# Optimization experiments

Hardware: AMD Instinct MI355X
Metric: run time of the kernel (lower is better)

Reference implementation:

```python
import jax, jax.numpy as jnp
import numpy as np

B, OBS, H, N = 16384, 512, 1024, 9

def setup_inputs() -> dict:
    key = jax.random.key(0)
    ks = jax.random.split(key, 12)
    s = 0.02
    return {
        "obs": jax.random.normal(ks[0], (B, OBS), jnp.float32),
        "agent_positions": jax.random.normal(ks[1], (B, N, 3), jnp.float32),
        "W1": jax.random.normal(ks[2], (OBS, H), jnp.float32) * s,
        "b1": jnp.zeros((H,), jnp.float32),
        "W2": jax.random.normal(ks[3], (H, H), jnp.float32) * s,
        "b2": jnp.zeros((H,), jnp.float32),
        "Wc1": jax.random.normal(ks[4], (H, H // 2), jnp.float32) * s,
        "bc1": jnp.zeros((H // 2,), jnp.float32),
        "Wc2": jax.random.normal(ks[5], (H // 2, 1), jnp.float32) * s,
        "bc2": jnp.zeros((1,), jnp.float32),
        "Wt1": jax.random.normal(ks[6], (H, H // 2), jnp.float32) * s,
        "bt1": jnp.zeros((H // 2,), jnp.float32),
        "Wt2": jax.random.normal(ks[7], (H // 2, 1), jnp.float32) * s,
        "bt2": jnp.zeros((1,), jnp.float32),
        "Wk1": jax.random.normal(ks[8], (2 * H, H), jnp.float32) * s,
        "bk1": jnp.zeros((H,), jnp.float32),
        "Wk2": jax.random.normal(ks[9], (H, 1), jnp.float32) * s,
        "bk2": jnp.zeros((1,), jnp.float32),
    }


def reference(obs, agent_positions, W1, b1, W2, b2, Wc1, bc1, Wc2, bc2,
              Wt1, bt1, Wt2, bt2, Wk1, bk1, Wk2, bk2):
    # global features: Linear->ReLU->Linear->ReLU
    g = jax.nn.relu(obs @ W1 + b1)
    g = jax.nn.relu(g @ W2 + b2)  # [B, H]

    # Each per-agent head is applied to the SAME g in the original loop,
    # so one pass + broadcast is mathematically identical.
    cov = jax.nn.sigmoid(jax.nn.relu(g @ Wc1 + bc1) @ Wc2 + bc2)  # [B,1]
    trk = jax.nn.sigmoid(jax.nn.relu(g @ Wt1 + bt1) @ Wt2 + bt2)  # [B,1]
    coop_in = jnp.concatenate([g, g], axis=-1)                    # [B,2H]
    coop = jax.nn.sigmoid(jax.nn.relu(coop_in @ Wk1 + bk1) @ Wk2 + bk2)  # [B,1]
    # mean over 8 identical cooperation scores == the score itself

    coverage = jnp.broadcast_to(cov, (cov.shape[0], N))      # [B, N]
    tracking = jnp.broadcast_to(trk, (trk.shape[0], N))      # [B, N]
    cooperation = jnp.broadcast_to(coop, (coop.shape[0], N)) # [B, N]
    return (coverage, tracking, cooperation)
```

## Files before the change

kernel.cpp:

```cpp
#include <hip/hip_runtime.h>
#include <hip/hip_bf16.h>

#define B_ROWS 16384
#define OBS_D  512
#define H_D    1024
#define N_AG   9

typedef __attribute__((ext_vector_type(8))) short short8;
typedef __attribute__((ext_vector_type(4))) float floatx4;

__device__ __forceinline__ unsigned short f_to_bf_raw(float f) {
  union { float f; unsigned u; } c; c.f = f;
  unsigned u = c.u;
  u = u + 0x7FFF + ((u >> 16) & 1);
  return (unsigned short)(u >> 16);
}

__device__ __forceinline__ size_t frag_off(int n, int k, int KT32) {
  const int ft = (n >> 4) * KT32 + (k >> 5);
  const int ln = (n & 15) | (((k >> 3) & 3) << 4);
  return ((size_t)ft * 64 + ln) * 8 + (k & 7);
}

__global__ __launch_bounds__(256) void prep_all(
    const float* __restrict__ obs,
    const float* __restrict__ W1, const float* __restrict__ W2,
    const float* __restrict__ Wc1, const float* __restrict__ Wt1,
    const float* __restrict__ Wk1,
    const float* __restrict__ bc1, const float* __restrict__ bt1,
    const float* __restrict__ bk1,
    const float* __restrict__ Wc2, const float* __restrict__ Wt2,
    const float* __restrict__ Wk2,
    unsigned short* __restrict__ obs_bf,
    unsigned short* __restrict__ W1f, unsigned short* __restrict__ W2f,
    unsigned short* __restrict__ WHf,
    float* __restrict__ bias2048, float* __restrict__ w2cat) {
  __shared__ float t[32][33];
  const int bx  = blockIdx.x;
  const int tid = threadIdx.x;

  if (bx < 4096) {
    int i = (bx * 256 + tid) * 8;
    float4 a = *(const float4*)(obs + i);
    float4 b = *(const float4*)(obs + i + 4);
    short8 o;
    o[0] = (short)f_to_bf_raw(a.x); o[1] = (short)f_to_bf_raw(a.y);
    o[2] = (short)f_to_bf_raw(a.z); o[3] = (short)f_to_bf_raw(a.w);
    o[4] = (short)f_to_bf_raw(b.x); o[5] = (short)f_to_bf_raw(b.y);
    o[6] = (short)f_to_bf_raw(b.z); o[7] = (short)f_to_bf_raw(b.w);
    *(short8*)(obs_bf + i) = o;
    return;
  }

  const int tx = tid & 31;
  const int ty = tid >> 5;

  if (bx < 4608) {
    const int tt = bx - 4096;
    const int k0 = (tt & 15) * 32;
    const int n0 = (tt >> 4) * 32;
#pragma unroll
    for (int i = ty; i < 32; i += 8)
      t[i][tx] = W1[(size_t)(k0 + i) * 1024 + n0 + tx];
    __syncthreads();
#pragma unroll
    for (int i = ty; i < 32; i += 8)
      W1f[frag_off(n0 + i, k0 + tx, 16)] = f_to_bf_raw(t[tx][i]);
    return;
  }

  if (bx < 5632) {
    const int tt = bx - 4608;
    const int k0 = (tt & 31) * 32;
    const int n0 = (tt >> 5) * 32;
#pragma unroll
    for (int i = ty; i < 32; i += 8)
      t[i][tx] = W2[(size_t)(k0 + i) * 1024 + n0 + tx];
    __syncthreads();
#pragma unroll
    for (int i = ty; i < 32; i += 8)
      W2f[frag_off(n0 + i, k0 + tx, 32)] = f_to_bf_raw(t[tx][i]);
    return;
  }

  if (bx < 7680) {
    const int tt = bx - 5632;
    const int k0 = (tt & 31) * 32;
    const int n0 = (tt >> 5) * 32;
#pragma unroll
    for (int i = ty; i < 32; i += 8) {
      const int n = n0 + tx;
      float v;
      if (n0 < 512)
        v = Wc1[(size_t)(k0 + i) * 512 + n];
      else if (n0 < 1024)
        v = Wt1[(size_t)(k0 + i) * 512 + (n - 512)];
      else
        v = Wk1[(size_t)(k0 + i) * 1024 + (n - 1024)]
          + Wk1[(size_t)(k0 + i + 1024) * 1024 + (n - 1024)];
      t[i][tx] = v;
    }
    __syncthreads();
#pragma unroll
    for (int i = ty; i < 32; i += 8)
      WHf[frag_off(n0 + i, k0 + tx, 32)] = f_to_bf_raw(t[tx][i]);
    return;
  }

  {
    int n = (bx - 7680) * 256 + tid;
    float b, w;
    if (n < 512)       { b = bc1[n];        w = Wc2[n]; }
    else if (n < 1024) { b = bt1[n - 512];  w = Wt2[n - 512]; }
    else               { b = bk1[n - 1024]; w = Wk2[n - 1024]; }
    bias2048[n] = b;
    w2cat[n] = w;
  }
}

#define GLD_LDS(gp, lp)                                                        \
  __builtin_amdgcn_global_load_lds(                                            \
      (const __attribute__((address_space(1))) void*)(gp),                     \
      (__attribute__((address_space(3))) void*)(lp), 16, 0, 0)

#define SBAR_PINNED()                                                          \
  __builtin_amdgcn_sched_barrier(0);                                           \
  __builtin_amdgcn_s_barrier();                                                \
  __builtin_amdgcn_sched_barrier(0)

#define MFMA_BF16(a, b, c) __builtin_amdgcn_mfma_f32_16x16x32_bf16(a, b, c, 0, 0, 0)

#define GEMM_CORE_V10(ACC_DECL)                                                \
  __shared__ __align__(16) unsigned short As[3][256 * 64];          \
  const int tid  = threadIdx.x;                                                \
  const int lane = tid & 63;                                                   \
  const int wave = tid >> 6;                                         \
  const int m0 = blockIdx.x * 256;                                             \
  const int n0 = blockIdx.y * 256;                                             \
  const int wm = (wave & 1) * 128;                  \
  const int wn = (wave >> 1) * 64;                                             \
  const int fr = lane & 15;                                                    \
  const int fq = lane >> 4;                                                    \
  ACC_DECL;                                                                    \
  constexpr int KT   = K >> 6;                      \
  constexpr int KT32 = K >> 5;                      \
  const size_t rowb = (size_t)K * 2;                                           \
  const int srow8  = lane >> 3;                   \
  const int schunk = (lane & 7) ^ srow8;          \
  const char* gA = (const char*)A + (size_t)(m0 + wave * 32 + srow8) * rowb    \
                   + schunk * 16;                                              \
  const unsigned short* gB =                                                   \
      Bf + ((size_t)(((n0 + wn) >> 4) * KT32) * 64 + lane) * 8;                \
  const int fsA = (wm + fr) * 128;                                             \
  const int sl0 = ((fq)     ^ (fr & 7)) * 16;                                  \
  const int sl1 = ((4 + fq) ^ (fr & 7)) * 16;                                  \
  short8 FbP[2][2][4];                                                         \
        \
        \
  _Pragma("unroll")                                                            \
  for (int j = 0; j < 4; ++j)                                                  \
    GLD_LDS(gA + (size_t)j * 8 * rowb,                                         \
            (char*)&As[0][0] + wave * 4096 + lane * 16 + j * 1024);            \
  __builtin_amdgcn_sched_barrier(0);                                           \
  _Pragma("unroll")                                                            \
  for (int j = 0; j < 4; ++j)                                                  \
    GLD_LDS(gA + 128 + (size_t)j * 8 * rowb,                                   \
            (char*)&As[1][0] + wave * 4096 + lane * 16 + j * 1024);            \
  __builtin_amdgcn_sched_barrier(0);                                           \
  _Pragma("unroll")                                                            \
  for (int s = 0; s < 2; ++s)                                                  \
    _Pragma("unroll")                                                          \
    for (int ni = 0; ni < 4; ++ni)                                             \
      FbP[0][s][ni] = *(const short8*)(gB + ((size_t)ni * KT32 + s) * 512);    \
  __builtin_amdgcn_sched_barrier(0);                                           \
  asm volatile("s_waitcnt vmcnt(12)" ::: "memory");        \
  __builtin_amdgcn_s_barrier();                                                \
  __builtin_amdgcn_sched_barrier(0);                                           \
  _Pragma("unroll")                                                            \
  for (int t = 0; t < KT; ++t) {           \
    if (t + 2 < KT) {                      \
      char* d = (char*)&As[(t + 2) % 3][0] + wave * 4096 + lane * 16;          \
      const char* g = gA + (size_t)(t + 2) * 128;                              \
      _Pragma("unroll")                                                        \
      for (int j = 0; j < 4; ++j)                                              \
        GLD_LDS(g + (size_t)j * 8 * rowb, d + j * 1024);                       \
    }                                                                          \
    const char* bA = (const char*)&As[t % 3][0];                               \
    _Pragma("unroll")                                                          \
    for (int p = 0; p < 4; ++p) {           \
      short8 Fa00 = *(const short8*)(bA + fsA + (2 * p) * 2048     + sl0);     \
      short8 Fa01 = *(const short8*)(bA + fsA + (2 * p) * 2048     + sl1);     \
      short8 Fa10 = *(const short8*)(bA + fsA + (2 * p + 1) * 2048 + sl0);     \
      short8 Fa11 = *(const short8*)(bA + fsA + (2 * p + 1) * 2048 + sl1);     \
      if (t + 1 < KT) {                           \
        FbP[(t + 1) & 1][0][p] = *(const short8*)                              \
            (gB + ((size_t)p * KT32 + 2 * (t + 1)) * 512);                     \
        FbP[(t + 1) & 1][1][p] = *(const short8*)                              \
            (gB + ((size_t)p * KT32 + 2 * (t + 1) + 1) * 512);                 \
      }                                                                        \
      SBAR_PINNED();                                                           \
      __builtin_amdgcn_s_setprio(1);                                           \
      _Pragma("unroll")                                                        \
      for (int ni = 0; ni < 4; ++ni) {                                         \
        acc[2 * p][ni]     = MFMA_BF16(Fa00, FbP[t & 1][0][ni], acc[2 * p][ni]);     \
        acc[2 * p][ni]     = MFMA_BF16(Fa01, FbP[t & 1][1][ni], acc[2 * p][ni]);     \
        acc[2 * p + 1][ni] = MFMA_BF16(Fa10, FbP[t & 1][0][ni], acc[2 * p + 1][ni]); \
        acc[2 * p + 1][ni] = MFMA_BF16(Fa11, FbP[t & 1][1][ni], acc[2 * p + 1][ni]); \
      }                                                                        \
      __builtin_amdgcn_s_setprio(0);                                           \
      if (p < 3) { SBAR_PINNED(); }                                            \
    }                                                                          \
          \
          \
          \
    __builtin_amdgcn_sched_barrier(0);                                         \
    asm volatile("s_waitcnt vmcnt(12) lgkmcnt(0)" ::: "memory");               \
    __builtin_amdgcn_s_barrier();                                              \
    __builtin_amdgcn_sched_barrier(0);                                         \
  }

#define ACC_INIT                                                               \
  floatx4 acc[8][4];                                                           \
  _Pragma("unroll")                                                            \
  for (int i = 0; i < 8; ++i)                                                  \
    _Pragma("unroll")                                                          \
    for (int j = 0; j < 4; ++j) acc[i][j] = (floatx4){0.f, 0.f, 0.f, 0.f}

template <int K>
__global__ __launch_bounds__(512, 2) void gemm_bias_relu(
    const unsigned short* __restrict__ A,
    const unsigned short* __restrict__ Bf,
    const float* __restrict__ bias,
    unsigned short* __restrict__ C,
    int M, int N) {
  GEMM_CORE_V10(ACC_INIT)

#pragma unroll
  for (int ni = 0; ni < 4; ++ni) {
    const int gn = n0 + wn + ni * 16 + fr;
    const float bv = bias[gn];
#pragma unroll
    for (int mi = 0; mi < 8; ++mi) {
#pragma unroll
      for (int r = 0; r < 4; ++r) {
        const int gm = m0 + wm + mi * 16 + fq * 4 + r;
        float v = acc[mi][ni][r] + bv;
        v = v > 0.f ? v : 0.f;
        C[(size_t)gm * N + gn] = f_to_bf_raw(v);
      }
    }
  }
}

template <int K>
__global__ __launch_bounds__(512, 2) void gemm_heads_fused(
    const unsigned short* __restrict__ A,
    const unsigned short* __restrict__ Bf,
    const float* __restrict__ bias,
    const float* __restrict__ w2,
    float* __restrict__ part,
    int M, int N) {
  GEMM_CORE_V10(ACC_INIT)

  const int j = blockIdx.y * 4 + (wave >> 1);
  float w2v[4], bv[4];
#pragma unroll
  for (int ni = 0; ni < 4; ++ni) {
    const int gn = n0 + wn + ni * 16 + fr;
    w2v[ni] = w2[gn];
    bv[ni]  = bias[gn];
  }
#pragma unroll
  for (int mi = 0; mi < 8; ++mi) {
#pragma unroll
    for (int r = 0; r < 4; ++r) {
      float p = 0.f;
#pragma unroll
      for (int ni = 0; ni < 4; ++ni) {
        float v = acc[mi][ni][r] + bv[ni];
        v = v > 0.f ? v : 0.f;
        p += v * w2v[ni];
      }
      p += __shfl_xor(p, 1);
      p += __shfl_xor(p, 2);
      p += __shfl_xor(p, 4);
      p += __shfl_xor(p, 8);
      if (fr == 0) {
        const int gm = m0 + wm + mi * 16 + fq * 4 + r;
        part[(size_t)j * B_ROWS + gm] = p;
      }
    }
  }
}

__global__ __launch_bounds__(256) void final_out(
    const float* __restrict__ part,
    const float* __restrict__ bc2, const float* __restrict__ bt2,
    const float* __restrict__ bk2, float* __restrict__ out) {
  const int row = blockIdx.x * 256 + threadIdx.x;
  float sc = 0.f, st = 0.f, sk = 0.f;
#pragma unroll
  for (int j = 0; j < 8; ++j)  sc += part[(size_t)j * B_ROWS + row];
#pragma unroll
  for (int j = 8; j < 16; ++j) st += part[(size_t)j * B_ROWS + row];
#pragma unroll
  for (int j = 16; j < 32; ++j) sk += part[(size_t)j * B_ROWS + row];
  const float cv = 1.f / (1.f + expf(-(sc + bc2[0])));
  const float tv = 1.f / (1.f + expf(-(st + bt2[0])));
  const float kv = 1.f / (1.f + expf(-(sk + bk2[0])));
  float* o0 = out + (size_t)row * N_AG;
  float* o1 = out + (size_t)(B_ROWS + row) * N_AG;
  float* o2 = out + (size_t)(2 * B_ROWS + row) * N_AG;
#pragma unroll
  for (int a = 0; a < N_AG; ++a) { o0[a] = cv; o1[a] = tv; o2[a] = kv; }
}

extern "C" void kernel_launch(void* const* d_in, const int* in_sizes, int n_in,
                              void* d_out, int out_size, void* d_ws, size_t ws_size,
                              hipStream_t stream) {
  const float* obs = (const float*)d_in[0];
  const float* W1  = (const float*)d_in[2];
  const float* b1  = (const float*)d_in[3];
  const float* W2  = (const float*)d_in[4];
  const float* b2  = (const float*)d_in[5];
  const float* Wc1 = (const float*)d_in[6];
  const float* bc1 = (const float*)d_in[7];
  const float* Wc2 = (const float*)d_in[8];
  const float* bc2 = (const float*)d_in[9];
  const float* Wt1 = (const float*)d_in[10];
  const float* bt1 = (const float*)d_in[11];
  const float* Wt2 = (const float*)d_in[12];
  const float* bt2 = (const float*)d_in[13];
  const float* Wk1 = (const float*)d_in[14];
  const float* bk1 = (const float*)d_in[15];
  const float* Wk2 = (const float*)d_in[16];
  const float* bk2 = (const float*)d_in[17];
  float* out = (float*)d_out;

  char* ws = (char*)d_ws;
  const size_t MB = 1024 * 1024;
  const size_t FULL_NEED = 70 * MB + 16 * 1024;

  unsigned short *obs_bf, *W1f, *W2f, *WHf, *G1, *G;
  float *bias2048, *w2cat, *PART;
  const bool full = (ws_size == 0) || (ws_size >= FULL_NEED);

  if (full) {
    obs_bf   = (unsigned short*)(ws + 0);
    W1f      = (unsigned short*)(ws + 16 * MB);
    G        = (unsigned short*)(ws + 0);
    G1       = (unsigned short*)(ws + 32 * MB);
    PART     = (float*)(ws + 32 * MB);
    W2f      = (unsigned short*)(ws + 64 * MB);
    WHf      = (unsigned short*)(ws + 66 * MB);
    bias2048 = (float*)(ws + 70 * MB);
    w2cat    = (float*)(ws + 70 * MB + 8 * 1024);
  } else {
    obs_bf   = (unsigned short*)(ws + 0);
    G1       = (unsigned short*)(ws + 16 * MB);
    G        = (unsigned short*)(ws + 32 * MB);
    W1f      = (unsigned short*)(ws + 48 * MB);
    W2f      = (unsigned short*)(ws + 49 * MB);
    WHf      = (unsigned short*)(ws + 51 * MB);
    bias2048 = (float*)(ws + 55 * MB);
    w2cat    = (float*)(ws + 55 * MB + 8 * 1024);
    PART     = (float*)(ws + 55 * MB + 16 * 1024);
  }

  prep_all<<<7688, 256, 0, stream>>>(obs, W1, W2, Wc1, Wt1, Wk1,
                                     bc1, bt1, bk1, Wc2, Wt2, Wk2,
                                     obs_bf, W1f, W2f, WHf, bias2048, w2cat);

  if (full) {
    gemm_bias_relu<512><<<dim3(64, 4), 512, 0, stream>>>(
        obs_bf, W1f, b1, G1, B_ROWS, 1024);
    gemm_bias_relu<1024><<<dim3(64, 4), 512, 0, stream>>>(
        G1, W2f, b2, G, B_ROWS, 1024);
    gemm_heads_fused<1024><<<dim3(64, 8), 512, 0, stream>>>(
        G, WHf, bias2048, w2cat, PART, B_ROWS, 2048);
  } else {
    for (int h = 0; h < 2; ++h) {
      const size_t ro = (size_t)h * 8192;
      gemm_bias_relu<512><<<dim3(32, 4), 512, 0, stream>>>(
          obs_bf + ro * 512, W1f, b1, G1, 8192, 1024);
      gemm_bias_relu<1024><<<dim3(32, 4), 512, 0, stream>>>(
          G1, W2f, b2, G, 8192, 1024);
      gemm_heads_fused<1024><<<dim3(32, 8), 512, 0, stream>>>(
          G, WHf, bias2048, w2cat, PART + ro, 8192, 2048);
    }
  }

  final_out<<<B_ROWS / 256, 256, 0, stream>>>(PART, bc2, bt2, bk2, out);
}
```

Before: 262.1 us.

## Stage B tiles through LDS with double-buffered half-K phased pipeline

Reworks the GEMM main loop so that both A and the pre-fragmented B operand are loaded asynchronously into LDS through global_load_lds, instead of B being loaded from global straight into registers. The K tile is split into two 32-wide halves and four phases per iteration, each issuing the next stage's loads between barriers, with a two-buffer 128KB LDS layout. This is meant to cut register pressure and global B refetch latency and to overlap loads with MFMA more evenly. The cost is more barriers per iteration and a larger LDS footprint, which may limit occupancy.

```diff
diff --git a/kernel.cpp b/kernel.cpp
--- a/kernel.cpp
+++ b/kernel.cpp
@@ -123,15 +123,65 @@
       (const __attribute__((address_space(1))) void*)(gp),                     \
       (__attribute__((address_space(3))) void*)(lp), 16, 0, 0)
 
-#define SBAR_PINNED()                                                          \
-  __builtin_amdgcn_sched_barrier(0);                                           \
-  __builtin_amdgcn_s_barrier();                                                \
-  __builtin_amdgcn_sched_barrier(0)
+#define SCB __builtin_amdgcn_sched_barrier(0)
 
 #define MFMA_BF16(a, b, c) __builtin_amdgcn_mfma_f32_16x16x32_bf16(a, b, c, 0, 0, 0)
 
-#define GEMM_CORE_V10(ACC_DECL)                                                \
-  __shared__ __align__(16) unsigned short As[3][256 * 64];          \
+#define ST_A(T, kh)                                                            \
+  GLD_LDS(gA0 + (size_t)(T) * 128 + (kh) * 64,                                 \
+          Lds + ((T) & 1) * 65536 + (kh) * 16384 + lA0);                       \
+  GLD_LDS(gA1 + (size_t)(T) * 128 + (kh) * 64,                                 \
+          Lds + ((T) & 1) * 65536 + (kh) * 16384 + lA0 + 8192)
+
+#define ST_B(T, kh)                                                            \
+  GLD_LDS(gB0 + (size_t)(2 * (T) + (kh)) * 1024,                               \
+          Lds + ((T) & 1) * 65536 + (kh) * 16384 + lB0);                       \
+  GLD_LDS(gB1 + (size_t)(2 * (T) + (kh)) * 1024,                               \
+          Lds + ((T) & 1) * 65536 + (kh) * 16384 + lB0 + 8192)
+
+#define FB4(pb)                                                                \
+  Fb[0] = *(const short8*)((pb) + fbB);                                        \
+  Fb[1] = *(const short8*)((pb) + fbB + 1024);                                 \
+  Fb[2] = *(const short8*)((pb) + fbB + 2048);                                 \
+  Fb[3] = *(const short8*)((pb) + fbB + 3072)
+
+#define MFMA16(mh)                                                             \
+  acc[(mh)*4+0][0] = MFMA_BF16(Fa0, Fb[0], acc[(mh)*4+0][0]);                  \
+  acc[(mh)*4+0][1] = MFMA_BF16(Fa0, Fb[1], acc[(mh)*4+0][1]);                  \
+  acc[(mh)*4+0][2] = MFMA_BF16(Fa0, Fb[2], acc[(mh)*4+0][2]);                  \
+  acc[(mh)*4+0][3] = MFMA_BF16(Fa0, Fb[3], acc[(mh)*4+0][3]);                  \
+  acc[(mh)*4+1][0] = MFMA_BF16(Fa1, Fb[0], acc[(mh)*4+1][0]);                  \
+  acc[(mh)*4+1][1] = MFMA_BF16(Fa1, Fb[1], acc[(mh)*4+1][1]);                  \
+  acc[(mh)*4+1][2] = MFMA_BF16(Fa1, Fb[2], acc[(mh)*4+1][2]);                  \
+  acc[(mh)*4+1][3] = MFMA_BF16(Fa1, Fb[3], acc[(mh)*4+1][3]);                  \
+  acc[(mh)*4+2][0] = MFMA_BF16(Fa2, Fb[0], acc[(mh)*4+2][0]);                  \
+  acc[(mh)*4+2][1] = MFMA_BF16(Fa2, Fb[1], acc[(mh)*4+2][1]);                  \
+  acc[(mh)*4+2][2] = MFMA_BF16(Fa2, Fb[2], acc[(mh)*4+2][2]);                  \
+  acc[(mh)*4+2][3] = MFMA_BF16(Fa2, Fb[3], acc[(mh)*4+2][3]);                  \
+  acc[(mh)*4+3][0] = MFMA_BF16(Fa3, Fb[0], acc[(mh)*4+3][0]);                  \
+  acc[(mh)*4+3][1] = MFMA_BF16(Fa3, Fb[1], acc[(mh)*4+3][1]);                  \
+  acc[(mh)*4+3][2] = MFMA_BF16(Fa3, Fb[2], acc[(mh)*4+3][2]);                  \
+  acc[(mh)*4+3][3] = MFMA_BF16(Fa3, Fb[3], acc[(mh)*4+3][3])
+
+#define PHASE(TT, ks, mh, EXTRA_READS, STAGE_STMT, PRE_BAR2)                   \
+  {                                                                            \
+    const char* pb = Lds + ((TT) & 1) * 65536 + (ks) * 16384;                  \
+    short8 Fa0 = *(const short8*)(pb + faB + ((mh)*4+0)*1024);                 \
+    short8 Fa1 = *(const short8*)(pb + faB + ((mh)*4+1)*1024);                 \
+    short8 Fa2 = *(const short8*)(pb + faB + ((mh)*4+2)*1024);                 \
+    short8 Fa3 = *(const short8*)(pb + faB + ((mh)*4+3)*1024);                 \
+    EXTRA_READS;                                                               \
+    STAGE_STMT;                                                                \
+    SCB; __builtin_amdgcn_s_barrier(); SCB;                                    \
+    __builtin_amdgcn_s_setprio(1);                                             \
+    MFMA16(mh);                                                                \
+    __builtin_amdgcn_s_setprio(0);                                             \
+    PRE_BAR2;                                                                  \
+    SCB; __builtin_amdgcn_s_barrier(); SCB;                                    \
+  }
+
+#define GEMM_CORE_V12(ACC_DECL)                                                \
+  __shared__ __align__(16) char Lds[131072];                                   \
   const int tid  = threadIdx.x;                                                \
   const int lane = tid & 63;                                                   \
   const int wave = tid >> 6;                                         \
@@ -142,81 +192,45 @@
   const int fr = lane & 15;                                                    \
   const int fq = lane >> 4;                                                    \
   ACC_DECL;                                                                    \
-  constexpr int KT   = K >> 6;                      \
-  constexpr int KT32 = K >> 5;                      \
+  constexpr int KT   = K >> 6;                                                 \
+  constexpr int KT32 = K >> 5;                                                 \
   const size_t rowb = (size_t)K * 2;                                           \
-  const int srow8  = lane >> 3;                   \
-  const int schunk = (lane & 7) ^ srow8;          \
-  const char* gA = (const char*)A + (size_t)(m0 + wave * 32 + srow8) * rowb    \
-                   + schunk * 16;                                              \
-  const unsigned short* gB =                                                   \
-      Bf + ((size_t)(((n0 + wn) >> 4) * KT32) * 64 + lane) * 8;                \
-  const int fsA = (wm + fr) * 128;                                             \
-  const int sl0 = ((fq)     ^ (fr & 7)) * 16;                                  \
-  const int sl1 = ((4 + fq) ^ (fr & 7)) * 16;                                  \
-  short8 FbP[2][2][4];                                                         \
-        \
-        \
+   \
+  const char* gA0 = (const char*)A                                             \
+      + (size_t)(m0 + wave * 16 + (lane >> 2)) * rowb + (lane & 3) * 16;       \
+  const char* gA1 = gA0 + (size_t)128 * rowb;                                  \
+     \
+  const char* gB0 = (const char*)Bf                                            \
+      + ((size_t)((n0 >> 4) + wave) * KT32) * 1024 + lane * 16;                \
+  const char* gB1 = gB0 + (size_t)8 * KT32 * 1024;                             \
+  const int lA0 = wave * 1024 + lane * 16;                                     \
+  const int lB0 = 32768 + wave * 1024 + lane * 16;                             \
+  const int faB = (wm + fr) * 64 + fq * 16;                                    \
+  const int fbB = 32768 + ((wave >> 1) * 4) * 1024 + lane * 16;                \
+  short8 Fb[4];                                                                \
+              \
+  ST_A(0, 0); ST_B(0, 0); ST_A(0, 1); ST_B(0, 1);                              \
+  SCB;                                                                         \
+  ST_A(1, 0); ST_B(1, 0);                                                      \
+  SCB;                                                                         \
+  asm volatile("s_waitcnt vmcnt(4)" ::: "memory");       \
+  __builtin_amdgcn_s_barrier();                  \
+  SCB;                                                                         \
   _Pragma("unroll")                                                            \
-  for (int j = 0; j < 4; ++j)                                                  \
-    GLD_LDS(gA + (size_t)j * 8 * rowb,                                         \
-            (char*)&As[0][0] + wave * 4096 + lane * 16 + j * 1024);            \
-  __builtin_amdgcn_sched_barrier(0);                                           \
-  _Pragma("unroll")                                                            \
-  for (int j = 0; j < 4; ++j)                                                  \
-    GLD_LDS(gA + 128 + (size_t)j * 8 * rowb,                                   \
-            (char*)&As[1][0] + wave * 4096 + lane * 16 + j * 1024);            \
-  __builtin_amdgcn_sched_barrier(0);                                           \
-  _Pragma("unroll")                                                            \
-  for (int s = 0; s < 2; ++s)                                                  \
-    _Pragma("unroll")                                                          \
-    for (int ni = 0; ni < 4; ++ni)                                             \
-      FbP[0][s][ni] = *(const short8*)(gB + ((size_t)ni * KT32 + s) * 512);    \
-  __builtin_amdgcn_sched_barrier(0);                                           \
-  asm volatile("s_waitcnt vmcnt(12)" ::: "memory");        \
-  __builtin_amdgcn_s_barrier();                                                \
-  __builtin_amdgcn_sched_barrier(0);                                           \
-  _Pragma("unroll")                                                            \
-  for (int t = 0; t < KT; ++t) {           \
-    if (t + 2 < KT) {                      \
-      char* d = (char*)&As[(t + 2) % 3][0] + wave * 4096 + lane * 16;          \
-      const char* g = gA + (size_t)(t + 2) * 128;                              \
-      _Pragma("unroll")                                                        \
-      for (int j = 0; j < 4; ++j)                                              \
-        GLD_LDS(g + (size_t)j * 8 * rowb, d + j * 1024);                       \
-    }                                                                          \
-    const char* bA = (const char*)&As[t % 3][0];                               \
-    _Pragma("unroll")                                                          \
-    for (int p = 0; p < 4; ++p) {           \
-      short8 Fa00 = *(const short8*)(bA + fsA + (2 * p) * 2048     + sl0);     \
-      short8 Fa01 = *(const short8*)(bA + fsA + (2 * p) * 2048     + sl1);     \
-      short8 Fa10 = *(const short8*)(bA + fsA + (2 * p + 1) * 2048 + sl0);     \
-      short8 Fa11 = *(const short8*)(bA + fsA + (2 * p + 1) * 2048 + sl1);     \
-      if (t + 1 < KT) {                           \
-        FbP[(t + 1) & 1][0][p] = *(const short8*)                              \
-            (gB + ((size_t)p * KT32 + 2 * (t + 1)) * 512);                     \
-        FbP[(t + 1) & 1][1][p] = *(const short8*)                              \
-            (gB + ((size_t)p * KT32 + 2 * (t + 1) + 1) * 512);                 \
-      }                                                                        \
-      SBAR_PINNED();                                                           \
-      __builtin_amdgcn_s_setprio(1);                                           \
-      _Pragma("unroll")                                                        \
-      for (int ni = 0; ni < 4; ++ni) {                                         \
-        acc[2 * p][ni]     = MFMA_BF16(Fa00, FbP[t & 1][0][ni], acc[2 * p][ni]);     \
-        acc[2 * p][ni]     = MFMA_BF16(Fa01, FbP[t & 1][1][ni], acc[2 * p][ni]);     \
-        acc[2 * p + 1][ni] = MFMA_BF16(Fa10, FbP[t & 1][0][ni], acc[2 * p + 1][ni]); \
-        acc[2 * p + 1][ni] = MFMA_BF16(Fa11, FbP[t & 1][1][ni], acc[2 * p + 1][ni]); \
-      }                                                                        \
-      __builtin_amdgcn_s_setprio(0);                                           \
-      if (p < 3) { SBAR_PINNED(); }                                            \
-    }                                                                          \
-          \
-          \
-          \
-    __builtin_amdgcn_sched_barrier(0);                                         \
-    asm volatile("s_waitcnt vmcnt(12) lgkmcnt(0)" ::: "memory");               \
-    __builtin_amdgcn_s_barrier();                                              \
-    __builtin_amdgcn_sched_barrier(0);                                         \
+  for (int T = 0; T < KT; ++T) {           \
+    PHASE(T, 0, 0, FB4(pb), if (T + 1 < KT) { ST_A(T + 1, 1); }, (void)0);     \
+    PHASE(T, 0, 1, (void)0, if (T + 1 < KT) { ST_B(T + 1, 1); }, (void)0);     \
+    PHASE(T, 1, 0, FB4(pb), if (T + 2 < KT) { ST_A(T + 2, 0); }, (void)0);     \
+    PHASE(T, 1, 1, (void)0, if (T + 2 < KT) { ST_B(T + 2, 0); },               \
+          if (T + 1 < KT) {                                                    \
+            SCB;                                                               \
+            if (T + 2 < KT) {                                                  \
+              asm volatile("s_waitcnt vmcnt(4)" ::: "memory");                 \
+            } else {                                                           \
+              asm volatile("s_waitcnt vmcnt(0)" ::: "memory");                 \
+            }                                                                  \
+            SCB;                                                               \
+          });                                                                  \
   }
 
 #define ACC_INIT                                                               \
@@ -233,7 +247,7 @@
     const float* __restrict__ bias,
     unsigned short* __restrict__ C,
     int M, int N) {
-  GEMM_CORE_V10(ACC_INIT)
+  GEMM_CORE_V12(ACC_INIT)
 
 #pragma unroll
   for (int ni = 0; ni < 4; ++ni) {
@@ -260,7 +274,7 @@
     const float* __restrict__ w2,
     float* __restrict__ part,
     int M, int N) {
-  GEMM_CORE_V10(ACC_INIT)
+  GEMM_CORE_V12(ACC_INIT)
 
   const int j = blockIdx.y * 4 + (wave >> 1);
   float w2v[4], bv[4];
```

New measurement: 257.9 us. No clear change (-1.6%).
